# Kernel optimization log

Hardware: AMD Instinct MI355X
Metric: run time of the kernel (lower is better)

The kernel has to match this reference:

```python
import jax, jax.numpy as jnp
import numpy as np

NZ, N_GEN = 128, 10
H1, H2, IMG = 512, 1024, 784
BATCH = 4096


def setup_inputs() -> dict:
    key = jax.random.key(0)
    ks = jax.random.split(key, 5)
    z = jax.random.normal(ks[0], (BATCH, NZ), dtype=jnp.float32)
    g_idx = jax.random.randint(ks[1], (BATCH,), 0, N_GEN)
    # stacked per-generator MLP weights (fan-in scaled init)
    W1 = jax.random.normal(ks[2], (N_GEN, NZ, H1), dtype=jnp.float32) / np.sqrt(NZ)
    b1 = jnp.zeros((N_GEN, H1), dtype=jnp.float32)
    W2 = jax.random.normal(ks[3], (N_GEN, H1, H2), dtype=jnp.float32) / np.sqrt(H1)
    b2 = jnp.zeros((N_GEN, H2), dtype=jnp.float32)
    W3 = jax.random.normal(ks[4], (N_GEN, H2, IMG), dtype=jnp.float32) / np.sqrt(H2)
    b3 = jnp.zeros((N_GEN, IMG), dtype=jnp.float32)
    return {"z": z, "g_idx": g_idx, "W1": W1, "b1": b1, "W2": W2, "b2": b2, "W3": W3, "b3": b3}


def reference(z, g_idx, W1, b1, W2, b2, W3, b3):
    # Run ALL n_gen sub-generators for every sample (as the torch module does),
    # then gather the chosen branch per sample.
    h = jax.nn.relu(jnp.einsum('bz,gzh->bgh', z, W1) + b1)          # [B, G, H1]
    h = jax.nn.relu(jnp.einsum('bgh,ghk->bgk', h, W2) + b2)         # [B, G, H2]
    images = jnp.tanh(jnp.einsum('bgk,gki->bgi', h, W3) + b3)       # [B, G, IMG]
    # images[arange(B), g_idx]
    out = jnp.take_along_axis(images, g_idx[:, None, None], axis=1)[:, 0]  # [B, IMG]
    return out
```

## Files before the change

### kernel.cpp

```cpp
#include <hip/hip_runtime.h>
#include <math.h>

#define NZ    128
#define H1    512
#define H2    1024
#define IMG   784
#define IMGP  832
#define BATCH 4096
#define NGEN  10
#define MPAD  128

typedef _Float16 f16;
typedef __attribute__((ext_vector_type(8))) _Float16 half8;
typedef __attribute__((ext_vector_type(4))) float floatx4;

__device__ __forceinline__ void cp16(void* l, const void* g) {
    __builtin_amdgcn_global_load_lds((const __attribute__((address_space(1))) void*)g,
                                     (__attribute__((address_space(3))) void*)l, 16, 0, 0);
}

__global__ __launch_bounds__(1024)
void hist_perm(const int* __restrict__ g_idx, int* __restrict__ seg,
               int* __restrict__ perm) {
    __shared__ int lc[NGEN];
    __shared__ int lb[NGEN + 1];
    const int t = threadIdx.x;
    if (t < NGEN) lc[t] = 0;
    __syncthreads();
    int gv[BATCH / 1024];
    #pragma unroll
    for (int i = 0; i < BATCH / 1024; ++i) {
        gv[i] = g_idx[t + i * 1024];
        atomicAdd(&lc[gv[i]], 1);
    }
    __syncthreads();
    if (t == 0) {
        int s = 0;
        for (int g = 0; g < NGEN; ++g) { lb[g] = s; s += lc[g]; }
        lb[NGEN] = s;
    }
    __syncthreads();
    if (t <= NGEN) seg[t] = lb[t];
    if (t < NGEN) lc[t] = lb[t];
    __syncthreads();
    #pragma unroll
    for (int i = 0; i < BATCH / 1024; ++i) {
        int p = atomicAdd(&lc[gv[i]], 1);
        perm[p] = t + i * 1024;
    }
}

__global__ void pack_z(const float* __restrict__ z, const int* __restrict__ perm,
                       f16* __restrict__ zp) {
    const int i = blockIdx.x * 256 + threadIdx.x;
    const int r = i >> 5, c = (i & 31) * 4;
    const int s = perm[r];
    float4 v = *(const float4*)(z + (size_t)s * NZ + c);
    union { ushort4 u; f16 h[4]; } o;
    o.h[0] = (f16)v.x; o.h[1] = (f16)v.y; o.h[2] = (f16)v.z; o.h[3] = (f16)v.w;
    *(ushort4*)(zp + (size_t)r * NZ + c) = o.u;
}

template<int K, int N, int NPAD>
__global__ __launch_bounds__(256)
void transpose_f16(const float* __restrict__ W, f16* __restrict__ Wt) {
    const int g  = blockIdx.z;
    const int k0 = blockIdx.x * 32;
    const int n0 = blockIdx.y * 32;
    __shared__ f16 L[32][36];
    const int t = threadIdx.x;
    {
        const int kk = t >> 3;
        const int nq = (t & 7) * 4;
        float4 v = make_float4(0.f, 0.f, 0.f, 0.f);
        if (n0 + nq < N)
            v = *(const float4*)(W + ((size_t)g * K + (k0 + kk)) * N + n0 + nq);
        L[nq + 0][kk] = (f16)v.x;
        L[nq + 1][kk] = (f16)v.y;
        L[nq + 2][kk] = (f16)v.z;
        L[nq + 3][kk] = (f16)v.w;
    }
    __syncthreads();
    {
        const int nn = t >> 3;
        const int kq = (t & 7) * 4;
        *(ushort4*)(Wt + ((size_t)g * NPAD + (n0 + nn)) * K + k0 + kq) =
            *(const ushort4*)&L[nn][kq];
    }
}

template<int K, int NOUT, int NPADB, int ACT, int SCATTER>
__global__ __launch_bounds__(256)
void gemm64(const f16* __restrict__ Ap, const f16* __restrict__ Wt,
            const float* __restrict__ bias, f16* __restrict__ Ch,
            float* __restrict__ Cout, const int* __restrict__ seg,
            const int* __restrict__ perm) {
    const int g  = blockIdx.z;
    const int s0 = seg[g];
    const int ng = seg[g + 1] - s0;
    const int m0 = blockIdx.x * 64;
    if (m0 >= ng) return;
    const int n0 = blockIdx.y * 64;

    __shared__ f16 As[64 * 64];
    __shared__ f16 Bs[64 * 64];

    const int tid = threadIdx.x, lane = tid & 63, w = tid >> 6;

    const f16* ga[2]; const f16* gb[2]; f16* la[2]; f16* lb[2];
    #pragma unroll
    for (int j = 0; j < 2; ++j) {
        const int r   = w * 16 + j * 8 + (lane >> 3);
        const int swz = ((lane & 7) ^ ((r >> 1) & 7)) * 8;
        ga[j] = Ap + (size_t)(s0 + m0 + r) * K + swz;
        gb[j] = Wt + ((size_t)g * NPADB + n0 + r) * K + swz;
        la[j] = As + (w * 16 + j * 8) * 64;
        lb[j] = Bs + (w * 16 + j * 8) * 64;
    }

    const int wm = (w & 1) * 32, wn = (w >> 1) * 32;
    const int lm = lane & 15, lq = lane >> 4;

    floatx4 acc[2][2] = {};

    #pragma unroll
    for (int kc = 0; kc < K / 64; ++kc) {
        __syncthreads();
        #pragma unroll
        for (int j = 0; j < 2; ++j) {
            cp16(la[j], ga[j]); cp16(lb[j], gb[j]);
            ga[j] += 64; gb[j] += 64;
        }
        __syncthreads();
        #pragma unroll
        for (int ks = 0; ks < 2; ++ks) {
            half8 a[2], b[2];
            #pragma unroll
            for (int mt = 0; mt < 2; ++mt) {
                const int r  = wm + mt * 16 + lm;
                const int pq = (ks * 4 + lq) ^ ((r >> 1) & 7);
                a[mt] = *(const half8*)&As[r * 64 + pq * 8];
            }
            #pragma unroll
            for (int nf = 0; nf < 2; ++nf) {
                const int r  = wn + 2 * lm + nf;
                const int pq = (ks * 4 + lq) ^ ((r >> 1) & 7);
                b[nf] = *(const half8*)&Bs[r * 64 + pq * 8];
            }
            #pragma unroll
            for (int mt = 0; mt < 2; ++mt)
                #pragma unroll
                for (int nf = 0; nf < 2; ++nf)
                    acc[mt][nf] = __builtin_amdgcn_mfma_f32_16x16x32_f16(
                        a[mt], b[nf], acc[mt][nf], 0, 0, 0);
        }
    }

    const int c = n0 + wn + 2 * lm;
    const float b0 = (c     < NOUT) ? bias[(size_t)g * NOUT + c]     : 0.f;
    const float b1 = (c + 1 < NOUT) ? bias[(size_t)g * NOUT + c + 1] : 0.f;
    #pragma unroll
    for (int mt = 0; mt < 2; ++mt)
        #pragma unroll
        for (int rr = 0; rr < 4; ++rr) {
            const int gr = m0 + wm + mt * 16 + lq * 4 + rr;
            if (gr >= ng) continue;
            float x0 = acc[mt][0][rr] + b0;
            float x1 = acc[mt][1][rr] + b1;
            if (ACT == 0) {
                x0 = fmaxf(x0, 0.f); x1 = fmaxf(x1, 0.f);
            } else {
                const float e0 = __expf(2.f * x0);
                const float e1 = __expf(2.f * x1);
                x0 = 1.f - 2.f / (e0 + 1.f);
                x1 = 1.f - 2.f / (e1 + 1.f);
            }
            if (SCATTER) {
                if (c < NOUT) {
                    const size_t orow = (size_t)perm[s0 + gr];
                    *(float2*)&Cout[orow * NOUT + c] = make_float2(x0, x1);
                }
            } else {
                union { uint u; f16 h[2]; } o;
                o.h[0] = (f16)x0; o.h[1] = (f16)x1;
                *(uint*)&Ch[(size_t)(s0 + gr) * NOUT + c] = o.u;
            }
        }
}

extern "C" void kernel_launch(void* const* d_in, const int* in_sizes, int n_in,
                              void* d_out, int out_size, void* d_ws, size_t ws_size,
                              hipStream_t stream) {
    const float* z    = (const float*)d_in[0];
    const int*   gidx = (const int*)  d_in[1];
    const float* W1   = (const float*)d_in[2];
    const float* b1   = (const float*)d_in[3];
    const float* W2   = (const float*)d_in[4];
    const float* b2   = (const float*)d_in[5];
    const float* W3   = (const float*)d_in[6];
    const float* b3   = (const float*)d_in[7];
    float* out = (float*)d_out;

    char* ws = (char*)d_ws;
    size_t off = 0;
    auto alloc = [&](size_t bytes) { size_t o = off; off = (off + bytes + 255) & ~255ULL; return o; };
    int* seg  = (int*)(ws + alloc((size_t)(NGEN + 1) * 4));
    int* perm = (int*)(ws + alloc((size_t)(BATCH + MPAD) * 4));
    f16* zp  = (f16*)(ws + alloc((size_t)(BATCH + MPAD) * NZ * 2));
    f16* h1p = (f16*)(ws + alloc((size_t)(BATCH + MPAD) * H1 * 2));
    f16* h2p = (f16*)(ws + alloc((size_t)(BATCH + MPAD) * H2 * 2));
    f16* W1t = (f16*)(ws + alloc((size_t)NGEN * H1 * NZ * 2));
    f16* W2t = (f16*)(ws + alloc((size_t)NGEN * H2 * H1 * 2));
    f16* W3t = (f16*)(ws + alloc((size_t)NGEN * IMGP * H2 * 2));

    hist_perm<<<dim3(1), dim3(1024), 0, stream>>>(gidx, seg, perm);
    pack_z<<<dim3(BATCH * (NZ / 4) / 256), dim3(256), 0, stream>>>(z, perm, zp);
    transpose_f16<NZ, H1, H1><<<dim3(NZ / 32, H1 / 32, NGEN), dim3(256), 0, stream>>>(W1, W1t);
    transpose_f16<H1, H2, H2><<<dim3(H1 / 32, H2 / 32, NGEN), dim3(256), 0, stream>>>(W2, W2t);
    transpose_f16<H2, IMG, IMGP><<<dim3(H2 / 32, IMGP / 32, NGEN), dim3(256), 0, stream>>>(W3, W3t);

    gemm64<NZ, H1, H1, 0, 0><<<dim3(16, H1 / 64, NGEN), dim3(256), 0, stream>>>(
        zp, W1t, b1, h1p, nullptr, seg, perm);
    gemm64<H1, H2, H2, 0, 0><<<dim3(16, H2 / 64, NGEN), dim3(256), 0, stream>>>(
        h1p, W2t, b2, h2p, nullptr, seg, perm);
    gemm64<H2, IMG, IMGP, 1, 1><<<dim3(16, IMGP / 64, NGEN), dim3(256), 0, stream>>>(
        h2p, W3t, b3, nullptr, out, seg, perm);
}
```

Baseline: 179.5 us.

## Merge prep kernels into one launch, fuse z gather, widen GEMM N tile

Combines the histogram/permutation pass and the three weight transposes into a single prep kernel, which cuts the launch count. The standalone pack_z kernel goes away: the first GEMM now gathers rows of z through perm and converts them to f16 directly into shared memory. GEMM tiles grow from 64x64 to 64x128, with each wave holding four accumulators, so weight reuse per block improves. In exchange the grid has fewer blocks, and IMGP is padded to 896, which adds wasted columns to the last layer.

```diff
diff --git a/kernel.cpp b/kernel.cpp
--- a/kernel.cpp
+++ b/kernel.cpp
@@ -5,7 +5,7 @@
 #define H1    512
 #define H2    1024
 #define IMG   784
-#define IMGP  832
+#define IMGP  896
 #define BATCH 4096
 #define NGEN  10
 #define MPAD  128
@@ -14,60 +14,23 @@
 typedef __attribute__((ext_vector_type(8))) _Float16 half8;
 typedef __attribute__((ext_vector_type(4))) float floatx4;
 
+#define NB1 ((NZ / 32) * (H1 / 32) * NGEN)
+#define NB2 ((H1 / 32) * (H2 / 32) * NGEN)
+#define NB3 ((H2 / 32) * (IMGP / 32) * NGEN)
+
 __device__ __forceinline__ void cp16(void* l, const void* g) {
     __builtin_amdgcn_global_load_lds((const __attribute__((address_space(1))) void*)g,
                                      (__attribute__((address_space(3))) void*)l, 16, 0, 0);
 }
 
-__global__ __launch_bounds__(1024)
-void hist_perm(const int* __restrict__ g_idx, int* __restrict__ seg,
-               int* __restrict__ perm) {
-    __shared__ int lc[NGEN];
-    __shared__ int lb[NGEN + 1];
-    const int t = threadIdx.x;
-    if (t < NGEN) lc[t] = 0;
-    __syncthreads();
-    int gv[BATCH / 1024];
-    #pragma unroll
-    for (int i = 0; i < BATCH / 1024; ++i) {
-        gv[i] = g_idx[t + i * 1024];
-        atomicAdd(&lc[gv[i]], 1);
-    }
-    __syncthreads();
-    if (t == 0) {
-        int s = 0;
-        for (int g = 0; g < NGEN; ++g) { lb[g] = s; s += lc[g]; }
-        lb[NGEN] = s;
-    }
-    __syncthreads();
-    if (t <= NGEN) seg[t] = lb[t];
-    if (t < NGEN) lc[t] = lb[t];
-    __syncthreads();
-    #pragma unroll
-    for (int i = 0; i < BATCH / 1024; ++i) {
-        int p = atomicAdd(&lc[gv[i]], 1);
-        perm[p] = t + i * 1024;
-    }
-}
-
-__global__ void pack_z(const float* __restrict__ z, const int* __restrict__ perm,
-                       f16* __restrict__ zp) {
-    const int i = blockIdx.x * 256 + threadIdx.x;
-    const int r = i >> 5, c = (i & 31) * 4;
-    const int s = perm[r];
-    float4 v = *(const float4*)(z + (size_t)s * NZ + c);
-    union { ushort4 u; f16 h[4]; } o;
-    o.h[0] = (f16)v.x; o.h[1] = (f16)v.y; o.h[2] = (f16)v.z; o.h[3] = (f16)v.w;
-    *(ushort4*)(zp + (size_t)r * NZ + c) = o.u;
-}
-
 template<int K, int N, int NPAD>
-__global__ __launch_bounds__(256)
-void transpose_f16(const float* __restrict__ W, f16* __restrict__ Wt) {
-    const int g  = blockIdx.z;
-    const int k0 = blockIdx.x * 32;
-    const int n0 = blockIdx.y * 32;
-    __shared__ f16 L[32][36];
+__device__ __forceinline__ void t_tile(int idx, const float* __restrict__ W,
+                                       f16* __restrict__ Wt, f16 (*L)[36]) {
+    constexpr int KT = K / 32, NT = NPAD / 32;
+    const int g  = idx / (KT * NT);
+    const int r2 = idx % (KT * NT);
+    const int k0 = (r2 % KT) * 32;
+    const int n0 = (r2 / KT) * 32;
     const int t = threadIdx.x;
     {
         const int kk = t >> 3;
@@ -89,52 +52,123 @@
     }
 }
 
-template<int K, int NOUT, int NPADB, int ACT, int SCATTER>
 __global__ __launch_bounds__(256)
-void gemm64(const f16* __restrict__ Ap, const f16* __restrict__ Wt,
-            const float* __restrict__ bias, f16* __restrict__ Ch,
-            float* __restrict__ Cout, const int* __restrict__ seg,
-            const int* __restrict__ perm) {
+void prep(const float* __restrict__ W1, const float* __restrict__ W2,
+          const float* __restrict__ W3, f16* __restrict__ W1t,
+          f16* __restrict__ W2t, f16* __restrict__ W3t,
+          const int* __restrict__ g_idx, int* __restrict__ seg,
+          int* __restrict__ perm) {
+    __shared__ f16 L[32][36];
+    __shared__ int lc[NGEN];
+    __shared__ int lb[NGEN + 1];
+    int bid = blockIdx.x;
+    if (bid == 0) {
+        const int t = threadIdx.x;
+        if (t < NGEN) lc[t] = 0;
+        __syncthreads();
+        int gv[BATCH / 256];
+        #pragma unroll
+        for (int i = 0; i < BATCH / 256; ++i) {
+            gv[i] = g_idx[t + i * 256];
+            atomicAdd(&lc[gv[i]], 1);
+        }
+        __syncthreads();
+        if (t == 0) {
+            int s = 0;
+            for (int g = 0; g < NGEN; ++g) { lb[g] = s; s += lc[g]; }
+            lb[NGEN] = s;
+        }
+        __syncthreads();
+        if (t <= NGEN) seg[t] = lb[t];
+        if (t < NGEN) lc[t] = lb[t];
+        __syncthreads();
+        #pragma unroll
+        for (int i = 0; i < BATCH / 256; ++i) {
+            int p = atomicAdd(&lc[gv[i]], 1);
+            perm[p] = t + i * 256;
+        }
+        return;
+    }
+    --bid;
+    if (bid < NB1) { t_tile<NZ, H1, H1>(bid, W1, W1t, L); return; }
+    bid -= NB1;
+    if (bid < NB2) { t_tile<H1, H2, H2>(bid, W2, W2t, L); return; }
+    bid -= NB2;
+    t_tile<H2, IMG, IMGP>(bid, W3, W3t, L);
+}
+
+template<int K, int NOUT, int NPADB, int ACT, int SCATTER, int GATHER>
+__global__ __launch_bounds__(256)
+void gemm(const f16* __restrict__ Ap, const float* __restrict__ Az,
+          const f16* __restrict__ Wt, const float* __restrict__ bias,
+          f16* __restrict__ Ch, float* __restrict__ Cout,
+          const int* __restrict__ seg, const int* __restrict__ perm) {
     const int g  = blockIdx.z;
     const int s0 = seg[g];
     const int ng = seg[g + 1] - s0;
     const int m0 = blockIdx.x * 64;
     if (m0 >= ng) return;
-    const int n0 = blockIdx.y * 64;
+    const int n0 = blockIdx.y * 128;
 
     __shared__ f16 As[64 * 64];
-    __shared__ f16 Bs[64 * 64];
+    __shared__ f16 Bs[128 * 64];
 
     const int tid = threadIdx.x, lane = tid & 63, w = tid >> 6;
 
-    const f16* ga[2]; const f16* gb[2]; f16* la[2]; f16* lb[2];
+    const f16* gb[4]; f16* lb[4];
+    #pragma unroll
+    for (int j = 0; j < 4; ++j) {
+        const int r   = w * 32 + j * 8 + (lane >> 3);
+        const int swz = ((lane & 7) ^ ((r >> 1) & 7)) * 8;
+        gb[j] = Wt + ((size_t)g * NPADB + n0 + r) * K + swz;
+        lb[j] = Bs + (w * 32 + j * 8) * 64;
+    }
+
+    const f16* ga[2]; f16* la[2];
+    const float* gz[2]; f16* aw[2];
     #pragma unroll
     for (int j = 0; j < 2; ++j) {
         const int r   = w * 16 + j * 8 + (lane >> 3);
         const int swz = ((lane & 7) ^ ((r >> 1) & 7)) * 8;
-        ga[j] = Ap + (size_t)(s0 + m0 + r) * K + swz;
-        gb[j] = Wt + ((size_t)g * NPADB + n0 + r) * K + swz;
         la[j] = As + (w * 16 + j * 8) * 64;
-        lb[j] = Bs + (w * 16 + j * 8) * 64;
-    }
-
-    const int wm = (w & 1) * 32, wn = (w >> 1) * 32;
+        if constexpr (GATHER != 0) {
+            const int pr = min(s0 + m0 + r, BATCH - 1);
+            gz[j] = Az + (size_t)perm[pr] * K + (lane & 7) * 8;
+            aw[j] = As + (size_t)r * 64 + swz;
+        } else {
+            ga[j] = Ap + (size_t)(s0 + m0 + r) * K + swz;
+        }
+    }
+
+    const int wm = (w & 1) * 32, wn = (w >> 1) * 64;
     const int lm = lane & 15, lq = lane >> 4;
 
-    floatx4 acc[2][2] = {};
+    floatx4 acc[2][4] = {};
 
     #pragma unroll
     for (int kc = 0; kc < K / 64; ++kc) {
         __syncthreads();
         #pragma unroll
-        for (int j = 0; j < 2; ++j) {
-            cp16(la[j], ga[j]); cp16(lb[j], gb[j]);
-            ga[j] += 64; gb[j] += 64;
+        for (int j = 0; j < 4; ++j) { cp16(lb[j], gb[j]); gb[j] += 64; }
+        if constexpr (GATHER != 0) {
+            #pragma unroll
+            for (int j = 0; j < 2; ++j) {
+                const float4 v0 = *(const float4*)(gz[j]);
+                const float4 v1 = *(const float4*)(gz[j] + 4);
+                gz[j] += 64;
+                half8 h;
+                h[0] = (f16)v0.x; h[1] = (f16)v0.y; h[2] = (f16)v0.z; h[3] = (f16)v0.w;
+                h[4] = (f16)v1.x; h[5] = (f16)v1.y; h[6] = (f16)v1.z; h[7] = (f16)v1.w;
+                *(half8*)aw[j] = h;
+            }
+        } else {
+            #pragma unroll
+            for (int j = 0; j < 2; ++j) { cp16(la[j], ga[j]); ga[j] += 64; }
         }
         __syncthreads();
         #pragma unroll
         for (int ks = 0; ks < 2; ++ks) {
-            half8 a[2], b[2];
+            half8 a[2], b[4];
             #pragma unroll
             for (int mt = 0; mt < 2; ++mt) {
                 const int r  = wm + mt * 16 + lm;
@@ -142,23 +176,28 @@
                 a[mt] = *(const half8*)&As[r * 64 + pq * 8];
             }
             #pragma unroll
-            for (int nf = 0; nf < 2; ++nf) {
-                const int r  = wn + 2 * lm + nf;
+            for (int nf = 0; nf < 4; ++nf) {
+                const int r  = wn + (nf >> 1) * 32 + 2 * lm + (nf & 1);
                 const int pq = (ks * 4 + lq) ^ ((r >> 1) & 7);
                 b[nf] = *(const half8*)&Bs[r * 64 + pq * 8];
             }
             #pragma unroll
             for (int mt = 0; mt < 2; ++mt)
                 #pragma unroll
-                for (int nf = 0; nf < 2; ++nf)
+                for (int nf = 0; nf < 4; ++nf)
                     acc[mt][nf] = __builtin_amdgcn_mfma_f32_16x16x32_f16(
                         a[mt], b[nf], acc[mt][nf], 0, 0, 0);
         }
     }
 
     const int c = n0 + wn + 2 * lm;
-    const float b0 = (c     < NOUT) ? bias[(size_t)g * NOUT + c]     : 0.f;
-    const float b1 = (c + 1 < NOUT) ? bias[(size_t)g * NOUT + c + 1] : 0.f;
+    const float* bg = bias + (size_t)g * NOUT;
+    const bool in0 = (!SCATTER) || (c < NOUT);
+    const bool in1 = (!SCATTER) || (c + 32 < NOUT);
+    const float b0 = in0 ? bg[c]      : 0.f;
+    const float b1 = in0 ? bg[c + 1]  : 0.f;
+    const float b2 = in1 ? bg[c + 32] : 0.f;
+    const float b3 = in1 ? bg[c + 33] : 0.f;
     #pragma unroll
     for (int mt = 0; mt < 2; ++mt)
         #pragma unroll
@@ -167,23 +206,31 @@
             if (gr >= ng) continue;
             float x0 = acc[mt][0][rr] + b0;
             float x1 = acc[mt][1][rr] + b1;
+            float x2 = acc[mt][2][rr] + b2;
+            float x3 = acc[mt][3][rr] + b3;
             if (ACT == 0) {
                 x0 = fmaxf(x0, 0.f); x1 = fmaxf(x1, 0.f);
+                x2 = fmaxf(x2, 0.f); x3 = fmaxf(x3, 0.f);
             } else {
                 const float e0 = __expf(2.f * x0);
                 const float e1 = __expf(2.f * x1);
+                const float e2 = __expf(2.f * x2);
+                const float e3 = __expf(2.f * x3);
                 x0 = 1.f - 2.f / (e0 + 1.f);
                 x1 = 1.f - 2.f / (e1 + 1.f);
+                x2 = 1.f - 2.f / (e2 + 1.f);
+                x3 = 1.f - 2.f / (e3 + 1.f);
             }
             if (SCATTER) {
-                if (c < NOUT) {
-                    const size_t orow = (size_t)perm[s0 + gr];
-                    *(float2*)&Cout[orow * NOUT + c] = make_float2(x0, x1);
-                }
+                const size_t orow = (size_t)perm[s0 + gr];
+                if (in0) *(float2*)&Cout[orow * NOUT + c]      = make_float2(x0, x1);
+                if (in1) *(float2*)&Cout[orow * NOUT + c + 32] = make_float2(x2, x3);
             } else {
-                union { uint u; f16 h[2]; } o;
-                o.h[0] = (f16)x0; o.h[1] = (f16)x1;
-                *(uint*)&Ch[(size_t)(s0 + gr) * NOUT + c] = o.u;
+                union { uint u; f16 h[2]; } o0, o1;
+                o0.h[0] = (f16)x0; o0.h[1] = (f16)x1;
+                o1.h[0] = (f16)x2; o1.h[1] = (f16)x3;
+                *(uint*)&Ch[(size_t)(s0 + gr) * NOUT + c]      = o0.u;
+                *(uint*)&Ch[(size_t)(s0 + gr) * NOUT + c + 32] = o1.u;
             }
         }
 }
@@ -206,23 +253,19 @@
     auto alloc = [&](size_t bytes) { size_t o = off; off = (off + bytes + 255) & ~255ULL; return o; };
     int* seg  = (int*)(ws + alloc((size_t)(NGEN + 1) * 4));
     int* perm = (int*)(ws + alloc((size_t)(BATCH + MPAD) * 4));
-    f16* zp  = (f16*)(ws + alloc((size_t)(BATCH + MPAD) * NZ * 2));
     f16* h1p = (f16*)(ws + alloc((size_t)(BATCH + MPAD) * H1 * 2));
     f16* h2p = (f16*)(ws + alloc((size_t)(BATCH + MPAD) * H2 * 2));
     f16* W1t = (f16*)(ws + alloc((size_t)NGEN * H1 * NZ * 2));
     f16* W2t = (f16*)(ws + alloc((size_t)NGEN * H2 * H1 * 2));
     f16* W3t = (f16*)(ws + alloc((size_t)NGEN * IMGP * H2 * 2));
 
-    hist_perm<<<dim3(1), dim3(1024), 0, stream>>>(gidx, seg, perm);
-    pack_z<<<dim3(BATCH * (NZ / 4) / 256), dim3(256), 0, stream>>>(z, perm, zp);
-    transpose_f16<NZ, H1, H1><<<dim3(NZ / 32, H1 / 32, NGEN), dim3(256), 0, stream>>>(W1, W1t);
-    transpose_f16<H1, H2, H2><<<dim3(H1 / 32, H2 / 32, NGEN), dim3(256), 0, stream>>>(W2, W2t);
-    transpose_f16<H2, IMG, IMGP><<<dim3(H2 / 32, IMGP / 32, NGEN), dim3(256), 0, stream>>>(W3, W3t);
-
-    gemm64<NZ, H1, H1, 0, 0><<<dim3(16, H1 / 64, NGEN), dim3(256), 0, stream>>>(
-        zp, W1t, b1, h1p, nullptr, seg, perm);
-    gemm64<H1, H2, H2, 0, 0><<<dim3(16, H2 / 64, NGEN), dim3(256), 0, stream>>>(
-        h1p, W2t, b2, h2p, nullptr, seg, perm);
-    gemm64<H2, IMG, IMGP, 1, 1><<<dim3(16, IMGP / 64, NGEN), dim3(256), 0, stream>>>(
-        h2p, W3t, b3, nullptr, out, seg, perm);
-}
+    prep<<<dim3(1 + NB1 + NB2 + NB3), dim3(256), 0, stream>>>(
+        W1, W2, W3, W1t, W2t, W3t, gidx, seg, perm);
+
+    gemm<NZ, H1, H1, 0, 0, 1><<<dim3(16, H1 / 128, NGEN), dim3(256), 0, stream>>>(
+        nullptr, z, W1t, b1, h1p, nullptr, seg, perm);
+    gemm<H1, H2, H2, 0, 0, 0><<<dim3(16, H2 / 128, NGEN), dim3(256), 0, stream>>>(
+        h1p, nullptr, W2t, b2, h2p, nullptr, seg, perm);
+    gemm<H2, IMG, IMGP, 1, 1, 0><<<dim3(16, IMGP / 128, NGEN), dim3(256), 0, stream>>>(
+        h2p, nullptr, W3t, b3, nullptr, out, seg, perm);
+}
```

Result: faster. 173.5 us (-3.3%).
